# Performance work log

Hardware: AMD Instinct MI355X
Metric: run time of the kernel (lower is better)

Reference implementation:

```python
import jax, jax.numpy as jnp
import numpy as np

NUM_EMBEDDINGS = 1024
EMBEDDING_DIM = 256
COMMITMENT_COST = 0.25
EMA_DECAY = 0.99
EPSILON = 1e-10


def setup_inputs() -> dict:
    key = jax.random.key(0)
    k1, k2, k3 = jax.random.split(key, 3)
    z_e = jax.random.normal(k1, (32, EMBEDDING_DIM, 32, 32), dtype=jnp.float32)
    embedding = jax.random.normal(k2, (NUM_EMBEDDINGS, EMBEDDING_DIM), dtype=jnp.float32)
    ema_cluster_size = jnp.zeros((NUM_EMBEDDINGS,), dtype=jnp.float32)
    ema_w = jax.random.normal(k3, (NUM_EMBEDDINGS, EMBEDDING_DIM), dtype=jnp.float32)
    return {"z_e": z_e, "embedding": embedding,
            "ema_cluster_size": ema_cluster_size, "ema_w": ema_w}


def reference(z_e, embedding, ema_cluster_size, ema_w):
    B, C, H, W = z_e.shape
    K = embedding.shape[0]
    # [B,C,H,W] -> [B,H,W,C] -> [N,C]
    z_bhwc = jnp.transpose(z_e, (0, 2, 3, 1))
    z_flat = z_bhwc.reshape(-1, C)
    N = z_flat.shape[0]

    # squared-L2 distances: ||z||^2 + ||e||^2 - 2 z e^T  -> [N, K]
    distances = (jnp.sum(z_flat * z_flat, axis=1, keepdims=True)
                 + jnp.sum(embedding * embedding, axis=1)
                 - 2.0 * z_flat @ embedding.T)
    indices = jnp.argmin(distances, axis=1)  # [N]

    quantized = embedding[indices].reshape(z_bhwc.shape)  # [B,H,W,C]

    # EMA codebook update (training path); segment_sum replaces one-hot matmul
    counts = jax.ops.segment_sum(jnp.ones((N,), dtype=z_flat.dtype), indices,
                                 num_segments=K)
    new_cluster_size = ema_cluster_size * EMA_DECAY + (1.0 - EMA_DECAY) * counts
    dw = jax.ops.segment_sum(z_flat, indices, num_segments=K)  # [K, C]
    new_ema_w = ema_w * EMA_DECAY + (1.0 - EMA_DECAY) * dw
    n = jnp.sum(new_cluster_size)
    cluster_size = (new_cluster_size + EPSILON) / (n + K * EPSILON) * n
    new_embedding = new_ema_w / cluster_size[:, None]

    loss = COMMITMENT_COST * jnp.mean(
        (jax.lax.stop_gradient(quantized) - z_bhwc) ** 2)
    # straight-through estimator
    q_st = z_bhwc + jax.lax.stop_gradient(quantized - z_bhwc)

    avg_probs = counts / N
    perplexity = jnp.exp(-jnp.sum(avg_probs * jnp.log(avg_probs + 1e-10)))

    q_out = jnp.transpose(q_st, (0, 3, 1, 2))  # [B,C,H,W]
    token_map = indices.reshape(B, H, W)
    return (q_out, loss, perplexity, token_map,
            new_cluster_size, new_ema_w, new_embedding)
```

## Files before the change

kernel.cpp:

```cpp
#include <hip/hip_runtime.h>

#define C_DIM   256
#define HWN     1024
#define N_TOT   32768
#define NELEM   8388608
#define CHW     (C_DIM*HWN)
#define BIGF    3.4e38f
#define FLAG_CAP 8192
#define MARGIN  0.02f

typedef __attribute__((ext_vector_type(8)))  short bf16x8;
typedef __attribute__((ext_vector_type(16))) float f32x16;


__device__ inline unsigned short bf16_rne(float x) {
    unsigned int u = __float_as_uint(x);
    unsigned int r = (u + 0x7FFF + ((u >> 16) & 1)) >> 16;
    return (unsigned short)r;
}
__device__ inline float bf16_to_f(unsigned short h) {
    return __uint_as_float(((unsigned int)h) << 16);
}

__global__ __launch_bounds__(256)
void vq_eprep(const float* __restrict__ e, unsigned short* __restrict__ ebt) {
    const int t = threadIdx.x;
    const int ct = blockIdx.x;
    const int cg = blockIdx.y;
    const int u = t >> 5;
    const int row = t & 31;
    const float* src = e + (size_t)(ct*32 + row)*C_DIM + cg*64 + u*8;
    const float4 v0 = *(const float4*)(src);
    const float4 v1 = *(const float4*)(src + 4);
    const float xs[8] = {v0.x,v0.y,v0.z,v0.w,v1.x,v1.y,v1.z,v1.w};
    __align__(16) unsigned short hi[8], lo[8];
    #pragma unroll
    for (int j = 0; j < 8; j++) {
        hi[j] = bf16_rne(xs[j]);
        lo[j] = bf16_rne(xs[j] - bf16_to_f(hi[j]));
    }
    const int cs = cg*4 + (u >> 1);
    const int lpos = (u & 1)*32 + row;
    unsigned short* dhi = ebt + ((size_t)(ct*2 + 0)*16 + cs)*512 + lpos*8;
    unsigned short* dlo = ebt + ((size_t)(ct*2 + 1)*16 + cs)*512 + lpos*8;
    *(uint4*)dhi = *(const uint4*)hi;
    *(uint4*)dlo = *(const uint4*)lo;
}

__global__ void vq_enorm(const float* __restrict__ e, float* __restrict__ enorm) {
    const int t = threadIdx.x;
    const int w = t >> 6;
    const int lane = t & 63;
    const int k = blockIdx.x * 4 + w;
    const float4 v = *(const float4*)(e + (size_t)k * C_DIM + lane * 4);
    float s = fmaf(v.x, v.x, fmaf(v.y, v.y, fmaf(v.z, v.z, v.w * v.w)));
    #pragma unroll
    for (int off = 32; off > 0; off >>= 1) s += __shfl_down(s, off, 64);
    if (lane == 0) enorm[k] = s;
}

__global__ __launch_bounds__(256)
void vq_zprep(const float* __restrict__ z, unsigned short* __restrict__ zbt) {
    const int t = threadIdx.x;
    const int rt = blockIdx.x;
    const int cg = blockIdx.y;
    const int u = t >> 5;
    const int row = t & 31;
    const int n = rt*32 + row;
    const int b = n >> 10, p = n & 1023;
    const float* zb = z + (size_t)b*CHW + p;
    const int c0 = cg*64 + u*8;
    float xs[8];
    #pragma unroll
    for (int j = 0; j < 8; j++) xs[j] = zb[(size_t)(c0 + j)*HWN];
    __align__(16) unsigned short hi[8], lo[8];
    #pragma unroll
    for (int j = 0; j < 8; j++) {
        hi[j] = bf16_rne(xs[j]);
        lo[j] = bf16_rne(xs[j] - bf16_to_f(hi[j]));
    }
    const int cs = cg*4 + (u >> 1);
    const int lpos = (u & 1)*32 + row;
    unsigned short* base = zbt + (size_t)rt*16384;
    *(uint4*)(base + (0*16 + cs)*512 + lpos*8) = *(const uint4*)hi;
    *(uint4*)(base + (16   + cs)*512 + lpos*8) = *(const uint4*)lo;
}

__global__ __launch_bounds__(256, 2)
void vq_argmin_mfma(const unsigned short* __restrict__ zbt,
                    const unsigned short* __restrict__ ebt,
                    const float* __restrict__ enorm,
                    int* __restrict__ idx_arr, int* __restrict__ counts_i,
                    int* __restrict__ flag_cnt, int* __restrict__ flags) {
    __shared__ __align__(16) unsigned short eslab[16384];
    __shared__ float redd[64][2];
    __shared__ float reds[64][2];
    __shared__ int   redi[64][2];

    const int t = threadIdx.x;
    const int lane = t & 63;
    const int w = t >> 6;
    const int rg = w >> 1;
    const int cg = w & 1;
    const int col = lane & 31;
    const int h = lane >> 5;
    const int n0 = blockIdx.x * 64;
    const int rt = (n0 >> 5) + rg;

    bf16x8 Ahi[16], Alo[16];
    const unsigned short* abase = zbt + (size_t)rt * 16384;
    #pragma unroll
    for (int cs = 0; cs < 16; cs++) {
        Ahi[cs] = *(const bf16x8*)(abase + (0*16 + cs)*512 + lane*8);
        Alo[cs] = *(const bf16x8*)(abase + (16   + cs)*512 + lane*8);
    }

    float bestd[16], secondd[16];
    int   besti[16];
    #pragma unroll
    for (int r = 0; r < 16; r++) { bestd[r] = BIGF; secondd[r] = BIGF; besti[r] = 0x7fffffff; }

    const int piece = t >> 6;
    const int tl = t & 63;

    for (int kc = 0; kc < 16; kc++) {
        f32x16 acc = {0,0,0,0,0,0,0,0,0,0,0,0,0,0,0,0};
        #pragma unroll
        for (int ph = 0; ph < 2; ph++) {
            __syncthreads();
            {
                const int lt = piece >> 1, pl = piece & 1;
                const int ct = kc*2 + lt;
                const unsigned short* src = ebt + ((size_t)(ct*2 + pl)*16 + ph*8)*512 + tl*8;
                unsigned short* dst = eslab + (size_t)piece*4096 + tl*8;
                #pragma unroll
                for (int r = 0; r < 8; r++)
                    *(uint4*)(dst + r*512) = *(const uint4*)(src + r*512);
            }
            __syncthreads();
            #pragma unroll
            for (int csl = 0; csl < 8; csl++) {
                const int cs = ph*8 + csl;
                const bf16x8 bh = *(const bf16x8*)(eslab + ((cg*2 + 0)*8 + csl)*512 + lane*8);
                const bf16x8 bl = *(const bf16x8*)(eslab + ((cg*2 + 1)*8 + csl)*512 + lane*8);
                acc = __builtin_amdgcn_mfma_f32_32x32x16_bf16(Ahi[cs], bh, acc, 0, 0, 0);
                acc = __builtin_amdgcn_mfma_f32_32x32x16_bf16(Ahi[cs], bl, acc, 0, 0, 0);
                acc = __builtin_amdgcn_mfma_f32_32x32x16_bf16(Alo[cs], bh, acc, 0, 0, 0);
            }
        }
        const int code = kc*64 + cg*32 + col;
        const float en = enorm[code];
        #pragma unroll
        for (int r = 0; r < 16; r++) {
            const float d = fmaf(-2.0f, acc[r], en);
            if (d < bestd[r]) { secondd[r] = bestd[r]; bestd[r] = d; besti[r] = code; }
            else if (d < secondd[r]) secondd[r] = d;
        }
    }

    #pragma unroll
    for (int m = 1; m < 32; m <<= 1) {
        #pragma unroll
        for (int r = 0; r < 16; r++) {
            const float od = __shfl_xor(bestd[r],   m, 64);
            const int   oi = __shfl_xor(besti[r],   m, 64);
            const float os = __shfl_xor(secondd[r], m, 64);
            const bool take = (od < bestd[r]) || (od == bestd[r] && oi < besti[r]);
            const float ns = take ? fminf(bestd[r], os) : fminf(secondd[r], od);
            if (take) { bestd[r] = od; besti[r] = oi; }
            secondd[r] = ns;
        }
    }
    __syncthreads();
    if (col == 0) {
        #pragma unroll
        for (int r = 0; r < 16; r++) {
            const int row = (r & 3) + 8*(r >> 2) + 4*h;
            redd[rg*32 + row][cg] = bestd[r];
            redi[rg*32 + row][cg] = besti[r];
            reds[rg*32 + row][cg] = secondd[r];
        }
    }
    __syncthreads();
    if (t < 64) {
        const float d0 = redd[t][0], d1 = redd[t][1];
        const int   i0 = redi[t][0], i1 = redi[t][1];
        const float s0 = reds[t][0], s1 = reds[t][1];
        const bool take = (d1 < d0) || (d1 == d0 && i1 < i0);
        const float bd = take ? d1 : d0;
        const int   bi = take ? i1 : i0;
        const float sd = take ? fminf(d0, s1) : fminf(s0, d1);
        const int n = n0 + t;
        idx_arr[n] = bi;
        atomicAdd(&counts_i[bi], 1);
        if (sd - bd < MARGIN) {
            const int pos = atomicAdd(flag_cnt, 1);
            if (pos < FLAG_CAP) flags[pos] = n;
        }
    }
}

__global__ __launch_bounds__(256)
void vq_fix(const float* __restrict__ z, const float* __restrict__ e,
            const float* __restrict__ enorm,
            const int* __restrict__ flag_cnt, const int* __restrict__ flags,
            int* __restrict__ idx_arr, int* __restrict__ counts_i) {
    __shared__ float zrow[256];
    __shared__ float rd[256];
    __shared__ int   ri[256];
    const int t = threadIdx.x;
    int cnt = *flag_cnt;
    if (cnt > FLAG_CAP) cnt = FLAG_CAP;
    for (int fi = blockIdx.x; fi < cnt; fi += (int)gridDim.x) {
        const int n = flags[fi];
        const int b = n >> 10, p = n & 1023;
        __syncthreads();
        zrow[t] = z[(size_t)b*CHW + (size_t)t*HWN + p];
        __syncthreads();
        float bd = BIGF; int bi = 0;
        for (int q = 0; q < 4; q++) {
            const int k = t*4 + q;
            const float* er = e + (size_t)k*C_DIM;
            float acc = 0.0f;
            for (int c = 0; c < C_DIM; c += 4) {
                const float4 ev = *(const float4*)(er + c);
                acc = fmaf(ev.x, zrow[c],   acc);
                acc = fmaf(ev.y, zrow[c+1], acc);
                acc = fmaf(ev.z, zrow[c+2], acc);
                acc = fmaf(ev.w, zrow[c+3], acc);
            }
            const float d = fmaf(-2.0f, acc, enorm[k]);
            if (d < bd) { bd = d; bi = k; }
        }
        rd[t] = bd; ri[t] = bi;
        __syncthreads();
        for (int s = 128; s > 0; s >>= 1) {
            if (t < s) {
                const float d2 = rd[t+s]; const int i2 = ri[t+s];
                if (d2 < rd[t] || (d2 == rd[t] && i2 < ri[t])) { rd[t] = d2; ri[t] = i2; }
            }
            __syncthreads();
        }
        if (t == 0) {
            const int old = idx_arr[n];
            if (ri[0] != old) {
                idx_arr[n] = ri[0];
                atomicAdd(&counts_i[old], -1);
                atomicAdd(&counts_i[ri[0]], 1);
            }
        }
        __syncthreads();
    }
}

__global__ void vq_scan_small(const int* __restrict__ counts_i,
                              const float* __restrict__ ema_cs,
                              float* __restrict__ out_perp,
                              float* __restrict__ out_ncs,
                              float* __restrict__ csize,
                              int* __restrict__ base, int* __restrict__ offs) {
    __shared__ float sf[1024];
    __shared__ int si[1024];
    const int t = threadIdx.x;
    const int ci = counts_i[t];
    const float cnt = (float)ci;
    const float ncs = ema_cs[t] * 0.99f + 0.01f * cnt;
    out_ncs[t] = ncs;

    sf[t] = ncs;
    __syncthreads();
    for (int s = 512; s > 0; s >>= 1) { if (t < s) sf[t] += sf[t + s]; __syncthreads(); }
    const float n_total = sf[0];
    __syncthreads();

    csize[t] = (ncs + 1e-10f) / (n_total + 1024.0f * 1e-10f) * n_total;

    const float pr = cnt * (1.0f / 32768.0f);
    sf[t] = pr * logf(pr + 1e-10f);
    __syncthreads();
    for (int s = 512; s > 0; s >>= 1) { if (t < s) sf[t] += sf[t + s]; __syncthreads(); }
    if (t == 0) out_perp[0] = expf(-sf[0]);

    si[t] = ci;
    __syncthreads();
    for (int d = 1; d < 1024; d <<= 1) {
        const int x = si[t];
        const int y = (t >= d) ? si[t - d] : 0;
        __syncthreads();
        si[t] = x + y;
        __syncthreads();
    }
    const int excl = si[t] - ci;
    base[t] = excl;
    offs[t] = excl;
}

__global__ __launch_bounds__(256)
void vq_scatter(const int* __restrict__ idx_arr, int* __restrict__ offs,
                int* __restrict__ order) {
    const int n = blockIdx.x * 256 + threadIdx.x;
    const int idx = idx_arr[n];
    const int pos = atomicAdd(&offs[idx], 1);
    order[pos] = n;
}

__global__ __launch_bounds__(256)
void vq_dw(const unsigned short* __restrict__ zbt, const int* __restrict__ order,
           const int* __restrict__ base, const int* __restrict__ counts_i,
           float* __restrict__ dw) {
    __shared__ int sord[1024];
    __shared__ float red[4][256];
    const int k = blockIdx.x;
    const int t = threadIdx.x;
    const int w = t >> 6;
    const int l = t & 63;
    const int plane = l >> 5;
    const int cs = (l >> 1) & 15;
    const int hh = l & 1;
    const int start = base[k];
    const int cnt = counts_i[k];
    const size_t loff = (size_t)(plane*16 + cs)*512 + hh*256;

    float acc[8] = {0,0,0,0,0,0,0,0};

    for (int s0 = 0; s0 < cnt; s0 += 1024) {
        const int m = min(1024, cnt - s0);
        __syncthreads();
        for (int i = t; i < m; i += 256) sord[i] = order[start + s0 + i];
        __syncthreads();
        const int mm = m & ~31;
        for (int g0 = w*8; g0 < mm; g0 += 32) {
            uint4 v[8];
            #pragma unroll
            for (int r = 0; r < 8; r++) {
                const int n = sord[g0 + r];
                const int rt = n >> 5, row = n & 31;
                v[r] = *(const uint4*)(zbt + (size_t)rt*16384 + loff + row*8);
            }
            #pragma unroll
            for (int r = 0; r < 8; r++) {
                const unsigned short* u = (const unsigned short*)&v[r];
                #pragma unroll
                for (int j = 0; j < 8; j++) acc[j] += bf16_to_f(u[j]);
            }
        }
        for (int i = mm + w; i < m; i += 4) {
            const int n = sord[i];
            const int rt = n >> 5, row = n & 31;
            const uint4 v = *(const uint4*)(zbt + (size_t)rt*16384 + loff + row*8);
            const unsigned short* u = (const unsigned short*)&v;
            #pragma unroll
            for (int j = 0; j < 8; j++) acc[j] += bf16_to_f(u[j]);
        }
    }

    #pragma unroll
    for (int j = 0; j < 8; j++) acc[j] += __shfl_xor(acc[j], 32, 64);
    if (l < 32) {
        #pragma unroll
        for (int j = 0; j < 8; j++) red[w][cs*16 + hh*8 + j] = acc[j];
    }
    __syncthreads();
    dw[(size_t)k*C_DIM + t] = red[0][t] + red[1][t] + red[2][t] + red[3][t];
}

__global__ __launch_bounds__(256)
void vq_combine(const float* __restrict__ z, const float* __restrict__ e,
                const int* __restrict__ idx_arr,
                float* __restrict__ loss_acc,
                float* __restrict__ qout, float* __restrict__ tokmap) {
    const int t = threadIdx.x;
    const int n = blockIdx.x * 256 + t;
    const int csplit = blockIdx.y;
    const int b = n >> 10, p = n & 1023;
    const int idx = idx_arr[n];
    if (csplit == 0) tokmap[n] = (float)idx;

    const float* zrow = z + (size_t)b*CHW + p;
    float* qrow = qout + (size_t)b*CHW + p;
    const float* erow = e + (size_t)idx*C_DIM;

    float lsum = 0.0f;
    for (int cc = 0; cc < 64; cc += 16) {
        const int cb = csplit*64 + cc;
        float ev[16];
        #pragma unroll
        for (int q4 = 0; q4 < 4; q4++) {
            const float4 v = *(const float4*)(erow + cb + q4*4);
            ev[q4*4+0] = v.x; ev[q4*4+1] = v.y; ev[q4*4+2] = v.z; ev[q4*4+3] = v.w;
        }
        #pragma unroll
        for (int j = 0; j < 16; j++) {
            const float zv = zrow[(size_t)(cb + j) * HWN];
            qrow[(size_t)(cb + j) * HWN] = ev[j];
            const float df = ev[j] - zv;
            lsum = fmaf(df, df, lsum);
        }
    }
    #pragma unroll
    for (int off = 32; off > 0; off >>= 1) lsum += __shfl_down(lsum, off, 64);
    __shared__ float ls[4];
    if ((t & 63) == 0) ls[t >> 6] = lsum;
    __syncthreads();
    if (t == 0) atomicAdd(loss_acc, ls[0] + ls[1] + ls[2] + ls[3]);
}

__global__ __launch_bounds__(256)
void vq_finalize_big(const float* __restrict__ ema_w, const float* __restrict__ dw,
                     const float* __restrict__ csize, const float* __restrict__ loss_acc,
                     float* __restrict__ out_ema_w, float* __restrict__ out_emb,
                     float* __restrict__ out_loss) {
    const int i4 = blockIdx.x * 256 + threadIdx.x;
    const int k = i4 >> 6;
    const float4 w = ((const float4*)ema_w)[i4];
    const float4 d = ((const float4*)dw)[i4];
    float4 nw;
    nw.x = fmaf(w.x, 0.99f, 0.01f * d.x);
    nw.y = fmaf(w.y, 0.99f, 0.01f * d.y);
    nw.z = fmaf(w.z, 0.99f, 0.01f * d.z);
    nw.w = fmaf(w.w, 0.99f, 0.01f * d.w);
    ((float4*)out_ema_w)[i4] = nw;
    const float cs = csize[k];
    float4 ne;
    ne.x = nw.x / cs; ne.y = nw.y / cs; ne.z = nw.z / cs; ne.w = nw.w / cs;
    ((float4*)out_emb)[i4] = ne;
    if (i4 == 0) out_loss[0] = 0.25f * loss_acc[0] * (1.0f / (float)NELEM);
}

extern "C" void kernel_launch(void* const* d_in, const int* in_sizes, int n_in,
                              void* d_out, int out_size, void* d_ws, size_t ws_size,
                              hipStream_t stream) {
    const float* z      = (const float*)d_in[0];
    const float* e      = (const float*)d_in[1];
    const float* ema_cs = (const float*)d_in[2];
    const float* ema_w  = (const float*)d_in[3];
    float* out = (float*)d_out;
    float* ws  = (float*)d_ws;

    int*   idx_arr  = (int*)ws;
    int*   flag_cnt = (int*)(ws + 32768);
    int*   counts_i = (int*)(ws + 32769);
    float* loss_acc = ws + 33793;
    int*   flags    = (int*)(ws + 33794);
    float* enorm    = ws + 41986;
    float* csize    = ws + 43010;
    int*   base     = (int*)(ws + 44034);
    int*   offs     = (int*)(ws + 45058);
    int*   order    = (int*)(ws + 46082);
    unsigned short* ebt = (unsigned short*)(ws + 78852);

    unsigned short* zbt = (unsigned short*)out;
    float* dw = out + 8684546;

    hipMemsetAsync(ws + 32768, 0, 4104, stream);

    vq_eprep<<<dim3(32, 4), 256, 0, stream>>>(e, ebt);
    vq_enorm<<<256, 256, 0, stream>>>(e, enorm);
    vq_zprep<<<dim3(1024, 4), 256, 0, stream>>>(z, zbt);
    vq_argmin_mfma<<<512, 256, 0, stream>>>(zbt, ebt, enorm, idx_arr, counts_i,
                                            flag_cnt, flags);
    vq_fix<<<64, 256, 0, stream>>>(z, e, enorm, flag_cnt, flags, idx_arr, counts_i);
    vq_scan_small<<<1, 1024, 0, stream>>>(counts_i, ema_cs,
                                          out + 8388609, out + 8421378, csize, base, offs);
    vq_scatter<<<128, 256, 0, stream>>>(idx_arr, offs, order);
    vq_dw<<<1024, 256, 0, stream>>>(zbt, order, base, counts_i, dw);
    vq_combine<<<dim3(128, 4), 256, 0, stream>>>(z, e, idx_arr, loss_acc,
                                                 out, out + 8388610);
    vq_finalize_big<<<256, 256, 0, stream>>>(ema_w, dw, csize, loss_acc,
                                             out + 8422402, out + 8684546,
                                             out + 8388608);
}
```

Before: 390.6 us.

## Load codebook MFMA fragments straight from global memory and write token map in argmin

The argmin MFMA kernel no longer stages codebook tiles through shared memory with two barriers per phase. Each wave now reads its bf16 hi/lo B fragments directly from the pre-laid-out codebook in global memory, relying on L2 to hold the 1 MB codebook. This removes the barriers and the LDS traffic and may allow more resident blocks. The cost is that the 2x reuse between the two row-group waves is lost, so L2 read traffic doubles. The token map float write also moves from the combine kernel into the argmin and fix kernels, so combine no longer writes it.

```diff
diff --git a/kernel.cpp b/kernel.cpp
--- a/kernel.cpp
+++ b/kernel.cpp
@@ -91,8 +91,8 @@
                     const unsigned short* __restrict__ ebt,
                     const float* __restrict__ enorm,
                     int* __restrict__ idx_arr, int* __restrict__ counts_i,
+                    float* __restrict__ tokmap,
                     int* __restrict__ flag_cnt, int* __restrict__ flags) {
-    __shared__ __align__(16) unsigned short eslab[16384];
     __shared__ float redd[64][2];
     __shared__ float reds[64][2];
     __shared__ int   redi[64][2];
@@ -120,33 +120,17 @@
     #pragma unroll
     for (int r = 0; r < 16; r++) { bestd[r] = BIGF; secondd[r] = BIGF; besti[r] = 0x7fffffff; }
 
-    const int piece = t >> 6;
-    const int tl = t & 63;
-
     for (int kc = 0; kc < 16; kc++) {
         f32x16 acc = {0,0,0,0,0,0,0,0,0,0,0,0,0,0,0,0};
-        #pragma unroll
-        for (int ph = 0; ph < 2; ph++) {
-            __syncthreads();
-            {
-                const int lt = piece >> 1, pl = piece & 1;
-                const int ct = kc*2 + lt;
-                const unsigned short* src = ebt + ((size_t)(ct*2 + pl)*16 + ph*8)*512 + tl*8;
-                unsigned short* dst = eslab + (size_t)piece*4096 + tl*8;
-                #pragma unroll
-                for (int r = 0; r < 8; r++)
-                    *(uint4*)(dst + r*512) = *(const uint4*)(src + r*512);
-            }
-            __syncthreads();
-            #pragma unroll
-            for (int csl = 0; csl < 8; csl++) {
-                const int cs = ph*8 + csl;
-                const bf16x8 bh = *(const bf16x8*)(eslab + ((cg*2 + 0)*8 + csl)*512 + lane*8);
-                const bf16x8 bl = *(const bf16x8*)(eslab + ((cg*2 + 1)*8 + csl)*512 + lane*8);
-                acc = __builtin_amdgcn_mfma_f32_32x32x16_bf16(Ahi[cs], bh, acc, 0, 0, 0);
-                acc = __builtin_amdgcn_mfma_f32_32x32x16_bf16(Ahi[cs], bl, acc, 0, 0, 0);
-                acc = __builtin_amdgcn_mfma_f32_32x32x16_bf16(Alo[cs], bh, acc, 0, 0, 0);
-            }
+        const unsigned short* bh_base = ebt + ((size_t)((kc*2 + cg)*2 + 0)*16)*512 + lane*8;
+        const unsigned short* bl_base = bh_base + (size_t)16*512;
+        #pragma unroll
+        for (int cs = 0; cs < 16; cs++) {
+            const bf16x8 bh = *(const bf16x8*)(bh_base + (size_t)cs*512);
+            const bf16x8 bl = *(const bf16x8*)(bl_base + (size_t)cs*512);
+            acc = __builtin_amdgcn_mfma_f32_32x32x16_bf16(Ahi[cs], bh, acc, 0, 0, 0);
+            acc = __builtin_amdgcn_mfma_f32_32x32x16_bf16(Ahi[cs], bl, acc, 0, 0, 0);
+            acc = __builtin_amdgcn_mfma_f32_32x32x16_bf16(Alo[cs], bh, acc, 0, 0, 0);
         }
         const int code = kc*64 + cg*32 + col;
         const float en = enorm[code];
@@ -192,6 +176,7 @@
         const float sd = take ? fminf(d0, s1) : fminf(s0, d1);
         const int n = n0 + t;
         idx_arr[n] = bi;
+        tokmap[n] = (float)bi;
         atomicAdd(&counts_i[bi], 1);
         if (sd - bd < MARGIN) {
             const int pos = atomicAdd(flag_cnt, 1);
@@ -204,7 +189,8 @@
 void vq_fix(const float* __restrict__ z, const float* __restrict__ e,
             const float* __restrict__ enorm,
             const int* __restrict__ flag_cnt, const int* __restrict__ flags,
-            int* __restrict__ idx_arr, int* __restrict__ counts_i) {
+            int* __restrict__ idx_arr, int* __restrict__ counts_i,
+            float* __restrict__ tokmap) {
     __shared__ float zrow[256];
     __shared__ float rd[256];
     __shared__ int   ri[256];
@@ -245,6 +231,7 @@
             const int old = idx_arr[n];
             if (ri[0] != old) {
                 idx_arr[n] = ri[0];
+                tokmap[n] = (float)ri[0];
                 atomicAdd(&counts_i[old], -1);
                 atomicAdd(&counts_i[ri[0]], 1);
             }
@@ -368,13 +355,12 @@
 void vq_combine(const float* __restrict__ z, const float* __restrict__ e,
                 const int* __restrict__ idx_arr,
                 float* __restrict__ loss_acc,
-                float* __restrict__ qout, float* __restrict__ tokmap) {
+                float* __restrict__ qout) {
     const int t = threadIdx.x;
     const int n = blockIdx.x * 256 + t;
     const int csplit = blockIdx.y;
     const int b = n >> 10, p = n & 1023;
     const int idx = idx_arr[n];
-    if (csplit == 0) tokmap[n] = (float)idx;
 
     const float* zrow = z + (size_t)b*CHW + p;
     float* qrow = qout + (size_t)b*CHW + p;
@@ -451,6 +437,7 @@
 
     unsigned short* zbt = (unsigned short*)out;
     float* dw = out + 8684546;
+    float* tokmap = out + 8388610;
 
     hipMemsetAsync(ws + 32768, 0, 4104, stream);
 
@@ -458,14 +445,14 @@
     vq_enorm<<<256, 256, 0, stream>>>(e, enorm);
     vq_zprep<<<dim3(1024, 4), 256, 0, stream>>>(z, zbt);
     vq_argmin_mfma<<<512, 256, 0, stream>>>(zbt, ebt, enorm, idx_arr, counts_i,
-                                            flag_cnt, flags);
-    vq_fix<<<64, 256, 0, stream>>>(z, e, enorm, flag_cnt, flags, idx_arr, counts_i);
+                                            tokmap, flag_cnt, flags);
+    vq_fix<<<64, 256, 0, stream>>>(z, e, enorm, flag_cnt, flags, idx_arr, counts_i,
+                                   tokmap);
     vq_scan_small<<<1, 1024, 0, stream>>>(counts_i, ema_cs,
                                           out + 8388609, out + 8421378, csize, base, offs);
     vq_scatter<<<128, 256, 0, stream>>>(idx_arr, offs, order);
     vq_dw<<<1024, 256, 0, stream>>>(zbt, order, base, counts_i, dw);
-    vq_combine<<<dim3(128, 4), 256, 0, stream>>>(z, e, idx_arr, loss_acc,
-                                                 out, out + 8388610);
+    vq_combine<<<dim3(128, 4), 256, 0, stream>>>(z, e, idx_arr, loss_acc, out);
     vq_finalize_big<<<256, 256, 0, stream>>>(ema_w, dw, csize, loss_acc,
                                              out + 8422402, out + 8684546,
                                              out + 8388608);
```

Measured after the change: 396.0 us. About the same (+1.4%).
